# Optimization experiments

Measured on AMD Instinct MI355X. Metric: run time of the kernel, lower is better.

Reference implementation:

```python
import jax, jax.numpy as jnp
import numpy as np

N_NODES = 200_000
N_EVENTS = 50_000
MEM = 128
RAW = 64
TD = 64
HEADS = 2
DH = MEM // HEADS
EDGE_DIM = RAW + TD
MSG_IN = 2 * MEM + RAW + TD


def _time_enc(x, w, b):
    # PyG TimeEncoder: cos(Linear(t)) with Linear(1, time_dim)
    return jnp.cos(x[..., None] * w + b)


def setup_inputs() -> dict:
    key = jax.random.key(0)
    ks = jax.random.split(key, 30)

    def w(i, shape, scale=None):
        s = scale if scale is not None else 1.0 / np.sqrt(shape[-1])
        return jax.random.normal(ks[i], shape, jnp.float32) * s

    src = jax.random.randint(ks[0], (N_EVENTS,), 0, N_NODES)
    dst = jax.random.randint(ks[1], (N_EVENTS,), 0, N_NODES)
    t = jnp.sort(jax.random.uniform(ks[2], (N_EVENTS,), jnp.float32, 0.0, 1e4))
    return dict(
        memory=w(3, (N_NODES, MEM), 1.0),
        last_update=jnp.zeros((N_NODES,), jnp.float32),
        t=t,
        msg=w(4, (N_EVENTS, RAW), 1.0),
        src=src, dst=dst,
        time_w=w(5, (TD,), 1.0), time_b=w(6, (TD,), 1.0),
        gru_Wih=w(7, (3 * MEM, MSG_IN)), gru_bih=w(8, (3 * MEM,), 0.02),
        gru_Whh=w(9, (3 * MEM, MEM)), gru_bhh=w(10, (3 * MEM,), 0.02),
        Wq=w(11, (MEM, MEM)), bq=w(12, (MEM,), 0.02),
        Wk=w(13, (MEM, MEM)), bk=w(14, (MEM,), 0.02),
        Wv=w(15, (MEM, MEM)), bv=w(16, (MEM,), 0.02),
        We=w(17, (MEM, EDGE_DIM)),
        Wskip=w(18, (MEM, MEM)), bskip=w(19, (MEM,), 0.02),
        Wls=w(20, (MEM, MEM)), bls=w(21, (MEM,), 0.02),
        Wld=w(22, (MEM, MEM)), bld=w(23, (MEM,), 0.02),
        Wlf=w(24, (1, MEM)), blf=w(25, (1,), 0.02),
    )


def reference(memory, last_update, t, msg, src, dst, time_w, time_b,
              gru_Wih, gru_bih, gru_Whh, gru_bhh,
              Wq, bq, Wk, bk, Wv, bv, We, Wskip, bskip,
              Wls, bls, Wld, bld, Wlf, blf):
    N, D = memory.shape
    E = src.shape[0]
    # --- 1. IdentityMessage: raw store for src side and dst side of each event ---
    dt_s = t - last_update[src]
    dt_d = t - last_update[dst]
    m_s = jnp.concatenate([memory[src], memory[dst], msg, _time_enc(dt_s, time_w, time_b)], -1)
    m_d = jnp.concatenate([memory[dst], memory[src], msg, _time_enc(dt_d, time_w, time_b)], -1)
    all_msg = jnp.concatenate([m_s, m_d], 0)        # [2E, MSG_IN]
    all_id = jnp.concatenate([src, dst], 0)         # [2E]
    all_t = jnp.concatenate([t, t], 0)              # [2E]
    # --- 2. LastAggregator: keep the latest message per target node ---
    pos = jnp.arange(2 * E, dtype=jnp.int32)
    last_pos = jnp.full((N,), -1, jnp.int32).at[all_id].max(pos)
    is_last = last_pos[all_id] == pos               # [2E], exactly one True per touched node
    # --- 3. GRUCell memory update (computed per message, scattered for the last one) ---
    h = memory[all_id]
    gi = all_msg @ gru_Wih.T + gru_bih
    gh = h @ gru_Whh.T + gru_bhh
    ir, iz, i_n = jnp.split(gi, 3, -1)
    hr, hz, h_n = jnp.split(gh, 3, -1)
    r = jax.nn.sigmoid(ir + hr)
    zg = jax.nn.sigmoid(iz + hz)
    n = jnp.tanh(i_n + r * h_n)
    h_new = (1.0 - zg) * n + zg * h
    memory_new = memory.at[all_id].add(jnp.where(is_last[:, None], h_new - h, 0.0))
    last_update_new = last_update.at[all_id].max(jnp.where(is_last, all_t, -jnp.inf))
    # --- 4. GraphAttentionEmbedding: TransformerConv(heads=2, edge_dim) in eval mode ---
    rel_t = last_update_new[src] - t
    edge_attr = jnp.concatenate([_time_enc(rel_t, time_w, time_b), msg], -1)  # [E, EDGE_DIM]
    e_proj = edge_attr @ We.T                                                  # [E, MEM]
    q = (memory_new @ Wq.T + bq).reshape(N, HEADS, DH)
    k = (memory_new[src] @ Wk.T + bk + e_proj).reshape(E, HEADS, DH)
    v = (memory_new[src] @ Wv.T + bv + e_proj).reshape(E, HEADS, DH)
    logit = jnp.einsum('ehd,ehd->eh', q[dst], k) / np.sqrt(DH).astype(np.float32)
    mx = jnp.full((N, HEADS), -jnp.inf, memory.dtype).at[dst].max(logit)
    a = jnp.exp(logit - mx[dst])
    denom = jax.ops.segment_sum(a, dst, num_segments=N)
    attn = a / denom[dst]                                                      # segment softmax over incoming edges
    out = jnp.zeros((N, HEADS, DH), memory.dtype).at[dst].add(attn[..., None] * v)
    z = out.reshape(N, D) + memory_new @ Wskip.T + bskip                       # root/skip connection
    # --- 5. LinkPredictor on event endpoints ---
    hlp = jax.nn.relu(z[src] @ Wls.T + bls + z[dst] @ Wld.T + bld)
    return hlp @ Wlf.T + blf                                                   # [E, 1]
```

## Files before the change

### kernel.cpp

```cpp
#include <hip/hip_runtime.h>
#include <math.h>

#define NN 200000
#define NE 50000
#define D 128

#define WGRU_SZ  196608
#define WATTN_SZ 147456
#define WSKP_SZ  16384
#define WLINK_SZ 32768

__device__ __forceinline__ float frcp_(float x) { return __builtin_amdgcn_rcpf(x); }
__device__ __forceinline__ float fsig_(float x) { return frcp_(1.f + __expf(-x)); }
__device__ __forceinline__ float ftanh_(float x) {
    float xc = fminf(fmaxf(x, -15.f), 15.f);
    float t = __expf(2.f * xc);
    return (t - 1.f) * frcp_(t + 1.f);
}

__device__ __forceinline__ unsigned short f2bf(float f) {
    unsigned int u = __float_as_uint(f);
    u = (u + 0x7fffu + ((u >> 16) & 1u)) >> 16;
    return (unsigned short)u;
}
__device__ __forceinline__ float bf2f(unsigned short b) {
    return __uint_as_float(((unsigned int)b) << 16);
}

typedef short bf16x8 __attribute__((ext_vector_type(8)));
typedef float f32x4  __attribute__((ext_vector_type(4)));

__global__ void k_initprep(const float* __restrict__ Wih, const float* __restrict__ Whh,
                           const float* __restrict__ Wk, const float* __restrict__ Wv,
                           const float* __restrict__ Wq, const float* __restrict__ We,
                           const float* __restrict__ Wskip,
                           const float* __restrict__ Wls, const float* __restrict__ Wld,
                           const int* __restrict__ src, const int* __restrict__ dst,
                           unsigned short* __restrict__ wgru,
                           unsigned short* __restrict__ wattn,
                           unsigned short* __restrict__ wskp,
                           unsigned short* __restrict__ wlink,
                           int* __restrict__ last_pos, int* __restrict__ count) {
    int idx = blockIdx.x * 256 + threadIdx.x;
    if (idx == 0) *count = 0;
    if (idx < 2 * NE) {
        int id = (idx < NE) ? src[idx] : dst[idx - NE];
        atomicMax(&last_pos[id], idx + 1);
    }
    if (idx >= 49152 + 36864 + 4096 + 8192) return;
    float4 v;
    unsigned short* dstp;
    int ncopies, stride;
    if (idx < 49152) {
        int n = idx / 96;
        int c = (idx - n * 96) * 4;
        if (n < 384) {
            v = *(const float4*)&Wih[n * 384 + c];
            if (n < 256 && c < 128) {
                const float4 w2 = *(const float4*)&Whh[n * 128 + c];
                v.x += w2.x; v.y += w2.y; v.z += w2.z; v.w += w2.w;
            }
        } else {
            if (c >= 128) return;
            v = *(const float4*)&Whh[(n - 128) * 128 + c];
        }
        dstp = &wgru[n * 384 + c]; ncopies = 8; stride = WGRU_SZ;
    } else if (idx < 49152 + 36864) {
        int i2 = idx - 49152;
        int n = i2 / 96;
        int c = (i2 - n * 96) * 4;
        if (n < 256) {
            const float* Wm = (n < 128) ? Wk : Wv;
            int nn = n & 127;
            if (c < 128)       v = *(const float4*)&Wm[nn * 128 + c];
            else if (c < 256)  v = *(const float4*)&We[nn * 128 + (c - 128)];
            else return;
        } else {
            if (c < 256) return;
            v = *(const float4*)&Wq[(n - 256) * 128 + (c - 256)];
        }
        dstp = &wattn[n * 384 + c]; ncopies = 4; stride = WATTN_SZ;
    } else if (idx < 49152 + 36864 + 4096) {
        int i3 = idx - 49152 - 36864;
        int n = i3 / 32;
        int c = (i3 - n * 32) * 4;
        v = *(const float4*)&Wskip[n * 128 + c];
        dstp = &wskp[n * 128 + c]; ncopies = 8; stride = WSKP_SZ;
    } else {
        int i4 = idx - 49152 - 36864 - 4096;
        int n = i4 / 64;
        int c = (i4 - n * 64) * 4;
        if (c < 128) v = *(const float4*)&Wls[n * 128 + c];
        else         v = *(const float4*)&Wld[n * 128 + (c - 128)];
        dstp = &wlink[n * 256 + c]; ncopies = 4; stride = WLINK_SZ;
    }
    ushort4 b;
    b.x = f2bf(v.x); b.y = f2bf(v.y); b.z = f2bf(v.z); b.w = f2bf(v.w);
    for (int r = 0; r < ncopies; ++r)
        *(ushort4*)(dstp + (size_t)r * stride) = b;
}

__global__ void k_compact(const int* __restrict__ src, const int* __restrict__ dst,
                          const int* __restrict__ last_pos,
                          int* __restrict__ count, int* __restrict__ clist,
                          int* __restrict__ node2slot, int* __restrict__ head) {
    int i = blockIdx.x * blockDim.x + threadIdx.x;
    if (i < 2 * NE) {
        int id = (i < NE) ? src[i] : dst[i - NE];
        if (last_pos[id] == i + 1) {
            int s = atomicAdd(count, 1);
            clist[s] = i;
            node2slot[id] = s;
            head[s] = -1;
        }
    }
}

#define GMB 64
__global__ __launch_bounds__(512) void k_gru(
    const float* __restrict__ memp, const float* __restrict__ lup,
    const float* __restrict__ tp, const float* __restrict__ msgp,
    const int* __restrict__ srcp, const int* __restrict__ dstp,
    const float* __restrict__ twp, const float* __restrict__ tbp,
    const int* __restrict__ clist,
    const unsigned short* __restrict__ wgru_all,
    const float* __restrict__ bih, const float* __restrict__ bhh,
    const unsigned short* __restrict__ wskp_all, const float* __restrict__ bskip,
    const int* __restrict__ countp,
    unsigned short* __restrict__ mem_new, unsigned short* __restrict__ zbf,
    float* __restrict__ lu_new)
{
    __shared__ alignas(16) unsigned short Xs[64][392];
    __shared__ int sid[64], sother[64], se[64];
    __shared__ float sdt[64];
    int cnt = *countp;
    int base = blockIdx.x * GMB;
    if (base >= cnt) return;
    int tid = threadIdx.x;
    const unsigned short* __restrict__ wgru = wgru_all + (size_t)(blockIdx.x & 7) * WGRU_SZ;
    const unsigned short* __restrict__ wskp = wskp_all + (size_t)(blockIdx.x & 7) * WSKP_SZ;

    if (tid < 64) {
        int ii = base + tid;
        bool valid = ii < cnt;
        int iw = clist[valid ? ii : (cnt - 1)];
        int e = (iw < NE) ? iw : (iw - NE);
        int id    = (iw < NE) ? srcp[e] : dstp[e];
        int oth   = (iw < NE) ? dstp[e] : srcp[e];
        sid[tid] = id; sother[tid] = oth; se[tid] = e;
        float tt = tp[e];
        float lu = lup[id];
        sdt[tid] = tt - lu;
        if (valid) lu_new[id] = fmaxf(lu, tt);
    }
    __syncthreads();
    {
        int m = tid >> 3, li = tid & 7;
        int id = sid[m], oth = sother[m], e = se[m];
        float dt = sdt[m];
        #pragma unroll
        for (int j = 0; j < 12; ++j) {
            int c4 = li + 8 * j;
            float4 v;
            if (c4 < 32)      v = *(const float4*)&memp[id * D + c4 * 4];
            else if (c4 < 64) v = *(const float4*)&memp[oth * D + (c4 - 32) * 4];
            else if (c4 < 80) v = *(const float4*)&msgp[e * 64 + (c4 - 64) * 4];
            else {
                int c0 = (c4 - 80) * 4;
                v.x = cosf(dt * twp[c0 + 0] + tbp[c0 + 0]);
                v.y = cosf(dt * twp[c0 + 1] + tbp[c0 + 1]);
                v.z = cosf(dt * twp[c0 + 2] + tbp[c0 + 2]);
                v.w = cosf(dt * twp[c0 + 3] + tbp[c0 + 3]);
            }
            ushort4 b;
            b.x = f2bf(v.x); b.y = f2bf(v.y); b.z = f2bf(v.z); b.w = f2bf(v.w);
            *(ushort4*)&Xs[m][c4 * 4] = b;
        }
    }
    __syncthreads();

    int lane = tid & 63, w = tid >> 6;
    int q = lane >> 4, l15 = lane & 15;
    int q8 = q * 8, w16 = w * 16;

    f32x4 acc[4][4];
    #pragma unroll
    for (int mt = 0; mt < 4; ++mt)
        #pragma unroll
        for (int g = 0; g < 4; ++g)
            acc[mt][g] = (f32x4)(0.0f);

#define GRU_STEP(NG)                                                                      \
    {                                                                                     \
        bf16x8 a[4];                                                                      \
        _Pragma("unroll")                                                                 \
        for (int mt = 0; mt < 4; ++mt) a[mt] = *(const bf16x8*)&Xs[mt * 16 + l15][k0 + q8]; \
        _Pragma("unroll")                                                                 \
        for (int g = 0; g < NG; ++g) {                                                    \
            const bf16x8 b = *(const bf16x8*)&wgru[(g * 128 + w16 + l15) * 384 + k0 + q8]; \
            _Pragma("unroll")                                                             \
            for (int mt = 0; mt < 4; ++mt)                                                \
                acc[mt][g] = __builtin_amdgcn_mfma_f32_16x16x32_bf16(a[mt], b, acc[mt][g], 0, 0, 0); \
        }                                                                                 \
    }

    #pragma unroll 2
    for (int ks = 0; ks < 4; ++ks) { int k0 = ks * 32; GRU_STEP(4) }
    #pragma unroll 2
    for (int ks = 4; ks < 12; ++ks) { int k0 = ks * 32; GRU_STEP(3) }
#undef GRU_STEP

    float nval[4][4];
    {
        int c = w16 + l15;
        float br  = bih[c]       + bhh[c];
        float bz  = bih[128 + c] + bhh[128 + c];
        float bin = bih[256 + c];
        float bhn = bhh[256 + c];
        #pragma unroll
        for (int mt = 0; mt < 4; ++mt) {
            #pragma unroll
            for (int reg = 0; reg < 4; ++reg) {
                int m = mt * 16 + q * 4 + reg;
                float r  = fsig_(acc[mt][0][reg] + br);
                float zg = fsig_(acc[mt][1][reg] + bz);
                float n  = ftanh_(acc[mt][2][reg] + bin + r * (acc[mt][3][reg] + bhn));
                float hv = bf2f(Xs[m][c]);
                nval[mt][reg] = (1.f - zg) * n + zg * hv;
            }
        }
    }

    __syncthreads();
    {
        int c = w16 + l15;
        #pragma unroll
        for (int mt = 0; mt < 4; ++mt)
            #pragma unroll
            for (int reg = 0; reg < 4; ++reg)
                Xs[mt * 16 + q * 4 + reg][c] = f2bf(nval[mt][reg]);
    }
    __syncthreads();

    {
        #pragma unroll
        for (int j = 0; j < 2; ++j) {
            int ch = tid + 512 * j;
            int m = ch >> 4, c8 = ch & 15;
            *(uint4*)&mem_new[(size_t)(base + m) * D + c8 * 8] = *(const uint4*)&Xs[m][c8 * 8];
        }
    }

    f32x4 acc2[4];
    #pragma unroll
    for (int mt = 0; mt < 4; ++mt) acc2[mt] = (f32x4)(0.0f);
    #pragma unroll
    for (int ks = 0; ks < 4; ++ks) {
        int k0 = ks * 32;
        bf16x8 a[4];
        #pragma unroll
        for (int mt = 0; mt < 4; ++mt) a[mt] = *(const bf16x8*)&Xs[mt * 16 + l15][k0 + q8];
        const bf16x8 b = *(const bf16x8*)&wskp[(w16 + l15) * 128 + k0 + q8];
        #pragma unroll
        for (int mt = 0; mt < 4; ++mt)
            acc2[mt] = __builtin_amdgcn_mfma_f32_16x16x32_bf16(a[mt], b, acc2[mt], 0, 0, 0);
    }
    __syncthreads();
    {
        int ch = w16 + l15;
        float b = bskip[ch];
        #pragma unroll
        for (int mt = 0; mt < 4; ++mt)
            #pragma unroll
            for (int reg = 0; reg < 4; ++reg)
                Xs[mt * 16 + q * 4 + reg][ch] = f2bf(acc2[mt][reg] + b);
    }
    __syncthreads();
    {
        #pragma unroll
        for (int j = 0; j < 2; ++j) {
            int ch = tid + 512 * j;
            int m = ch >> 4, c8 = ch & 15;
            *(uint4*)&zbf[(size_t)(base + m) * D + c8 * 8] = *(const uint4*)&Xs[m][c8 * 8];
        }
    }
}

#define AMB 32
__global__ __launch_bounds__(256) void k_attnA(
    const int* __restrict__ srcp, const int* __restrict__ dstp,
    const float* __restrict__ tp, const float* __restrict__ msgp,
    const float* __restrict__ twp, const float* __restrict__ tbp,
    const float* __restrict__ lu_new, const int* __restrict__ node2slot,
    const unsigned short* __restrict__ mem_new,
    const unsigned short* __restrict__ wattn_all,
    const float* __restrict__ bq, const float* __restrict__ bk, const float* __restrict__ bv,
    unsigned short* __restrict__ vbuf, float* __restrict__ abuf,
    int* __restrict__ head, int* __restrict__ next)
{
    __shared__ alignas(16) unsigned short Xs[32][392];
    unsigned short (*kLb)[136] = (unsigned short(*)[136])(&Xs[0][0]);
    unsigned short (*qLb)[136] = (unsigned short(*)[136])(&Xs[0][0] + 4352);
    __shared__ float sa[AMB][2];
    __shared__ int sslot[AMB], sdslot[AMB];
    __shared__ float srel[AMB];
    int tid = threadIdx.x;
    int e0 = blockIdx.x * AMB;
    const unsigned short* __restrict__ wattn = wattn_all + (size_t)(blockIdx.x & 3) * WATTN_SZ;
    {
        int gid = blockIdx.x * 256 + tid;
        if (gid < NE) {
            int sl = node2slot[dstp[gid]];
            next[gid] = atomicExch(&head[sl], gid);
        }
    }
    if (tid < AMB) {
        int e = e0 + tid; if (e >= NE) e = NE - 1;
        int s = srcp[e], dd = dstp[e];
        sslot[tid]  = node2slot[s];
        sdslot[tid] = node2slot[dd];
        srel[tid] = lu_new[s] - tp[e];
    }
    __syncthreads();
    {
        int m = tid >> 3, li = tid & 7;
        int e = e0 + m; if (e >= NE) e = NE - 1;
        int ssl = sslot[m], dsl = sdslot[m];
        float rel = srel[m];
        uint4* xrow = (uint4*)&Xs[m][0];
        const uint4* srow = (const uint4*)&mem_new[(size_t)ssl * D];
        const uint4* drow = (const uint4*)&mem_new[(size_t)dsl * D];
        #pragma unroll
        for (int j = 0; j < 2; ++j) {
            xrow[li + 8 * j]      = srow[li + 8 * j];
            xrow[32 + li + 8 * j] = drow[li + 8 * j];
        }
        {
            int c0 = li * 8;
            ushort4 lo, hi;
            lo.x = f2bf(cosf(rel * twp[c0 + 0] + tbp[c0 + 0]));
            lo.y = f2bf(cosf(rel * twp[c0 + 1] + tbp[c0 + 1]));
            lo.z = f2bf(cosf(rel * twp[c0 + 2] + tbp[c0 + 2]));
            lo.w = f2bf(cosf(rel * twp[c0 + 3] + tbp[c0 + 3]));
            hi.x = f2bf(cosf(rel * twp[c0 + 4] + tbp[c0 + 4]));
            hi.y = f2bf(cosf(rel * twp[c0 + 5] + tbp[c0 + 5]));
            hi.z = f2bf(cosf(rel * twp[c0 + 6] + tbp[c0 + 6]));
            hi.w = f2bf(cosf(rel * twp[c0 + 7] + tbp[c0 + 7]));
            *(ushort4*)&Xs[m][128 + c0]     = lo;
            *(ushort4*)&Xs[m][128 + c0 + 4] = hi;
        }
        {
            float4 a = *(const float4*)&msgp[e * 64 + li * 8];
            float4 b = *(const float4*)&msgp[e * 64 + li * 8 + 4];
            ushort4 lo, hi;
            lo.x = f2bf(a.x); lo.y = f2bf(a.y); lo.z = f2bf(a.z); lo.w = f2bf(a.w);
            hi.x = f2bf(b.x); hi.y = f2bf(b.y); hi.z = f2bf(b.z); hi.w = f2bf(b.w);
            *(ushort4*)&Xs[m][192 + li * 8]     = lo;
            *(ushort4*)&Xs[m][192 + li * 8 + 4] = hi;
        }
    }
    __syncthreads();

    int lane = tid & 63, w = tid >> 6;
    int q = lane >> 4, l15 = lane & 15;
    int q8 = q * 8;

    f32x4 acc[2][6];
    #pragma unroll
    for (int mt = 0; mt < 2; ++mt)
        #pragma unroll
        for (int jj = 0; jj < 6; ++jj) acc[mt][jj] = (f32x4)(0.0f);

    #pragma unroll 2
    for (int ks = 0; ks < 8; ++ks) {
        int k0 = ks * 32;
        const bf16x8 a0 = *(const bf16x8*)&Xs[l15][k0 + q8];
        const bf16x8 a1 = *(const bf16x8*)&Xs[16 + l15][k0 + q8];
        #pragma unroll
        for (int jj = 0; jj < 4; ++jj) {
            int nt = w + 4 * jj;
            const bf16x8 b = *(const bf16x8*)&wattn[(nt * 16 + l15) * 384 + k0 + q8];
            acc[0][jj] = __builtin_amdgcn_mfma_f32_16x16x32_bf16(a0, b, acc[0][jj], 0, 0, 0);
            acc[1][jj] = __builtin_amdgcn_mfma_f32_16x16x32_bf16(a1, b, acc[1][jj], 0, 0, 0);
        }
    }
    #pragma unroll 2
    for (int ks = 8; ks < 12; ++ks) {
        int k0 = ks * 32;
        const bf16x8 a0 = *(const bf16x8*)&Xs[l15][k0 + q8];
        const bf16x8 a1 = *(const bf16x8*)&Xs[16 + l15][k0 + q8];
        #pragma unroll
        for (int jj = 4; jj < 6; ++jj) {
            int nt = w + 4 * jj;
            const bf16x8 b = *(const bf16x8*)&wattn[(nt * 16 + l15) * 384 + k0 + q8];
            acc[0][jj] = __builtin_amdgcn_mfma_f32_16x16x32_bf16(a0, b, acc[0][jj], 0, 0, 0);
            acc[1][jj] = __builtin_amdgcn_mfma_f32_16x16x32_bf16(a1, b, acc[1][jj], 0, 0, 0);
        }
    }

    __syncthreads();

    float vreg[2][2][4];
    #pragma unroll
    for (int jj = 0; jj < 6; ++jj) {
        int nt = w + 4 * jj;
        int gate = nt >> 3;
        int ch = (nt & 7) * 16 + l15;
        float bias = (gate == 0) ? bk[ch] : (gate == 1) ? bv[ch] : bq[ch];
        #pragma unroll
        for (int mt = 0; mt < 2; ++mt)
            #pragma unroll
            for (int reg = 0; reg < 4; ++reg) {
                int m = mt * 16 + q * 4 + reg;
                float val = acc[mt][jj][reg] + bias;
                if (gate == 0)      kLb[m][ch] = f2bf(val);
                else if (gate == 2) qLb[m][ch] = f2bf(val);
                else                vreg[jj - 2][mt][reg] = val;
            }
    }
    __syncthreads();
    #pragma unroll
    for (int pr = 0; pr < 16; ++pr) {
        int p2 = pr * 4 + w;
        int m = p2 >> 1, h = p2 & 1;
        float prod = bf2f(qLb[m][h * 64 + lane]) * bf2f(kLb[m][h * 64 + lane]);
        #pragma unroll
        for (int off = 32; off; off >>= 1) prod += __shfl_down(prod, off);
        if (lane == 0) {
            float a = __expf(prod * 0.125f);
            sa[m][h] = a;
            if (e0 + m < NE) abuf[(e0 + m) * 2 + h] = a;
        }
    }
    __syncthreads();
    {
        unsigned short (*vL)[136] = qLb;
        #pragma unroll
        for (int jv = 0; jv < 2; ++jv) {
            int ch = w * 16 + jv * 64 + l15;
            int h = jv;
            #pragma unroll
            for (int mt = 0; mt < 2; ++mt)
                #pragma unroll
                for (int reg = 0; reg < 4; ++reg) {
                    int m = mt * 16 + q * 4 + reg;
                    vL[m][ch] = f2bf(sa[m][h] * vreg[jv][mt][reg]);
                }
        }
        __syncthreads();
        #pragma unroll
        for (int j = 0; j < 2; ++j) {
            int chunk = tid + 256 * j;
            int row = chunk >> 4, c8 = chunk & 15;
            if (e0 + row < NE)
                *(uint4*)&vbuf[(size_t)(e0 + row) * D + c8 * 8] = *(const uint4*)&vL[row][c8 * 8];
        }
    }
}

__global__ __launch_bounds__(256) void k_gather(
    const int* __restrict__ countp, const int* __restrict__ head,
    const int* __restrict__ next, const float* __restrict__ abuf,
    const unsigned short* __restrict__ vbuf, unsigned short* __restrict__ zbf)
{
    int cnt = *countp;
    int slot = blockIdx.x * 32 + (threadIdx.x >> 3);
    if (slot >= cnt) return;
    int li = threadIdx.x & 7;
    int c0 = li * 16;
    int h = li >> 2;
    float vsum[16];
    #pragma unroll
    for (int j = 0; j < 16; ++j) vsum[j] = 0.f;
    float asum = 0.f;
    for (int e = head[slot]; e != -1; e = next[e]) {
        asum += abuf[e * 2 + h];
        uint4 v0 = *(const uint4*)&vbuf[(size_t)e * D + c0];
        uint4 v1 = *(const uint4*)&vbuf[(size_t)e * D + c0 + 8];
        const unsigned short* pv0 = (const unsigned short*)&v0;
        const unsigned short* pv1 = (const unsigned short*)&v1;
        #pragma unroll
        for (int j = 0; j < 8; ++j) { vsum[j] += bf2f(pv0[j]); vsum[8 + j] += bf2f(pv1[j]); }
    }
    if (asum > 0.f) {
        float rr = frcp_(asum);
        uint4 z0 = *(const uint4*)&zbf[(size_t)slot * D + c0];
        uint4 z1 = *(const uint4*)&zbf[(size_t)slot * D + c0 + 8];
        const unsigned short* pz0 = (const unsigned short*)&z0;
        const unsigned short* pz1 = (const unsigned short*)&z1;
        unsigned short o[16];
        #pragma unroll
        for (int j = 0; j < 8; ++j) {
            o[j]     = f2bf(bf2f(pz0[j]) + vsum[j] * rr);
            o[8 + j] = f2bf(bf2f(pz1[j]) + vsum[8 + j] * rr);
        }
        *(uint4*)&zbf[(size_t)slot * D + c0]     = *(const uint4*)&o[0];
        *(uint4*)&zbf[(size_t)slot * D + c0 + 8] = *(const uint4*)&o[8];
    }
}

__global__ __launch_bounds__(256) void k_link(
    const int* __restrict__ srcp, const int* __restrict__ dstp,
    const int* __restrict__ node2slot,
    const unsigned short* __restrict__ zbf,
    const unsigned short* __restrict__ wlink_all,
    const float* __restrict__ bls, const float* __restrict__ bld,
    const float* __restrict__ Wlf, const float* __restrict__ blf,
    float* __restrict__ outp)
{
    __shared__ alignas(16) unsigned short Xs[32][264];
    __shared__ int ssl[32], sdl[32];
    __shared__ float sred[32][4];
    int tid = threadIdx.x;
    int e0 = blockIdx.x * 32;
    const unsigned short* __restrict__ wlink = wlink_all + (size_t)(blockIdx.x & 3) * WLINK_SZ;
    if (tid < 32) {
        int e = e0 + tid; if (e >= NE) e = NE - 1;
        ssl[tid] = node2slot[srcp[e]];
        sdl[tid] = node2slot[dstp[e]];
    }
    __syncthreads();
    {
        int m = tid >> 3, li = tid & 7;
        uint4* xrow = (uint4*)&Xs[m][0];
        const uint4* srow = (const uint4*)&zbf[(size_t)ssl[m] * D];
        const uint4* drow = (const uint4*)&zbf[(size_t)sdl[m] * D];
        xrow[li]      = srow[li];
        xrow[li + 8]  = srow[li + 8];
        xrow[16 + li] = drow[li];
        xrow[24 + li] = drow[li + 8];
    }
    __syncthreads();

    int lane = tid & 63, w = tid >> 6;
    int q = lane >> 4, l15 = lane & 15;
    int q8 = q * 8;

    f32x4 acc[2][2];
    #pragma unroll
    for (int mt = 0; mt < 2; ++mt)
        #pragma unroll
        for (int jj = 0; jj < 2; ++jj) acc[mt][jj] = (f32x4)(0.0f);

    #pragma unroll
    for (int ks = 0; ks < 8; ++ks) {
        int k0 = ks * 32;
        const bf16x8 a0 = *(const bf16x8*)&Xs[l15][k0 + q8];
        const bf16x8 a1 = *(const bf16x8*)&Xs[16 + l15][k0 + q8];
        #pragma unroll
        for (int jj = 0; jj < 2; ++jj) {
            int nt = w + 4 * jj;
            const bf16x8 b = *(const bf16x8*)&wlink[(nt * 16 + l15) * 256 + k0 + q8];
            acc[0][jj] = __builtin_amdgcn_mfma_f32_16x16x32_bf16(a0, b, acc[0][jj], 0, 0, 0);
            acc[1][jj] = __builtin_amdgcn_mfma_f32_16x16x32_bf16(a1, b, acc[1][jj], 0, 0, 0);
        }
    }

    float p[2][4];
    #pragma unroll
    for (int mt = 0; mt < 2; ++mt)
        #pragma unroll
        for (int reg = 0; reg < 4; ++reg) p[mt][reg] = 0.f;
    #pragma unroll
    for (int jj = 0; jj < 2; ++jj) {
        int ch = (w + 4 * jj) * 16 + l15;
        float bias = bls[ch] + bld[ch];
        float wl = Wlf[ch];
        #pragma unroll
        for (int mt = 0; mt < 2; ++mt)
            #pragma unroll
            for (int reg = 0; reg < 4; ++reg)
                p[mt][reg] += fmaxf(acc[mt][jj][reg] + bias, 0.f) * wl;
    }
    #pragma unroll
    for (int mask = 1; mask < 16; mask <<= 1) {
        #pragma unroll
        for (int mt = 0; mt < 2; ++mt)
            #pragma unroll
            for (int reg = 0; reg < 4; ++reg)
                p[mt][reg] += __shfl_xor(p[mt][reg], mask);
    }
    if (l15 == 0) {
        #pragma unroll
        for (int mt = 0; mt < 2; ++mt)
            #pragma unroll
            for (int reg = 0; reg < 4; ++reg)
                sred[mt * 16 + q * 4 + reg][w] = p[mt][reg];
    }
    __syncthreads();
    if (tid < 32) {
        int e = e0 + tid;
        if (e < NE)
            outp[e] = sred[tid][0] + sred[tid][1] + sred[tid][2] + sred[tid][3] + blf[0];
    }
}

extern "C" void kernel_launch(void* const* d_in, const int* in_sizes, int n_in,
                              void* d_out, int out_size, void* d_ws, size_t ws_size,
                              hipStream_t stream)
{
    const float* memory      = (const float*)d_in[0];
    const float* last_update = (const float*)d_in[1];
    const float* t           = (const float*)d_in[2];
    const float* msg         = (const float*)d_in[3];
    const int*   src         = (const int*)d_in[4];
    const int*   dst         = (const int*)d_in[5];
    const float* time_w      = (const float*)d_in[6];
    const float* time_b      = (const float*)d_in[7];
    const float* gru_Wih     = (const float*)d_in[8];
    const float* gru_bih     = (const float*)d_in[9];
    const float* gru_Whh     = (const float*)d_in[10];
    const float* gru_bhh     = (const float*)d_in[11];
    const float* Wq          = (const float*)d_in[12];
    const float* bq          = (const float*)d_in[13];
    const float* Wk          = (const float*)d_in[14];
    const float* bk          = (const float*)d_in[15];
    const float* Wv          = (const float*)d_in[16];
    const float* bv          = (const float*)d_in[17];
    const float* We          = (const float*)d_in[18];
    const float* Wskip       = (const float*)d_in[19];
    const float* bskip       = (const float*)d_in[20];
    const float* Wls         = (const float*)d_in[21];
    const float* bls         = (const float*)d_in[22];
    const float* Wld         = (const float*)d_in[23];
    const float* bld         = (const float*)d_in[24];
    const float* Wlf         = (const float*)d_in[25];
    const float* blf         = (const float*)d_in[26];
    float* outp = (float*)d_out;

    char* ws = (char*)d_ws;
    int*   last_pos  = (int*)  (ws + 0);
    int*   node2slot = (int*)  (ws + 800000);
    float* lu_new    = (float*)(ws + 1600000);
    int*   count     = (int*)  (ws + 2400000);
    int*   clist     = (int*)  (ws + 2400016);
    unsigned short* wgru    = (unsigned short*)(ws + 79624592);
    unsigned short* wattn   = (unsigned short*)(ws + 82770320);
    unsigned short* wskp    = (unsigned short*)(ws + 83949968);
    unsigned short* wlink   = (unsigned short*)(ws + 84212112);
    unsigned short* mem_new = (unsigned short*)(ws + 84474256);
    unsigned short* zbf     = (unsigned short*)(ws + 110082448);
    unsigned short* vbuf    = (unsigned short*)(ws + 135690640);
    float* abuf = (float*)(ws + 148490640);
    int*   head = (int*)  (ws + 148890640);
    int*   next = (int*)  (ws + 149290768);

    k_initprep<<<(2 * NE + 255) / 256, 256, 0, stream>>>(
                 gru_Wih, gru_Whh, Wk, Wv, Wq, We, Wskip, Wls, Wld, src, dst,
                 wgru, wattn, wskp, wlink, last_pos, count);
    k_compact <<<(2 * NE + 255) / 256, 256, 0, stream>>>(src, dst, last_pos, count,
                 clist, node2slot, head);
    k_gru     <<<(2 * NE + GMB - 1) / GMB, 512, 0, stream>>>(memory, last_update, t, msg,
                 src, dst, time_w, time_b, clist, wgru, gru_bih, gru_bhh,
                 wskp, bskip, count, mem_new, zbf, lu_new);
    k_attnA   <<<(NE + AMB - 1) / AMB, 256, 0, stream>>>(src, dst, t, msg, time_w, time_b,
                 lu_new, node2slot, mem_new, wattn, bq, bk, bv, vbuf, abuf, head, next);
    k_gather  <<<(2 * NE + 31) / 32, 256, 0, stream>>>(count, head, next, abuf, vbuf, zbf);
    k_link    <<<(NE + 31) / 32, 256, 0, stream>>>(src, dst, node2slot, zbf,
                 wlink, bls, bld, Wlf, blf, outp);
}
```

Before: 385.3 us.

## Precompute per-slot metadata and bf16 msg, widen attention tile to 64 edges

k_compact now writes a packed int4 per compacted slot (event, other node, dt, id) and the lu_new update, so k_gru no longer does a serial metadata phase with an extra barrier. msg is converted to bf16 once in k_initprep and both k_gru and k_attnA copy it directly. k_attnA is restructured to 64 edges per 512-thread block, with each wave owning one 16-channel column per gate, which increases A-fragment reuse per weight load. The cost is an extra msg conversion pass, a larger launch grid for initprep, and more LDS per attention block, which may lower occupancy.

```diff
diff --git a/kernel.cpp b/kernel.cpp
--- a/kernel.cpp
+++ b/kernel.cpp
@@ -9,6 +9,9 @@
 #define WATTN_SZ 147456
 #define WSKP_SZ  16384
 #define WLINK_SZ 32768
+
+#define CVT0 98304
+#define MSGB_V4 800000
 
 __device__ __forceinline__ float frcp_(float x) { return __builtin_amdgcn_rcpf(x); }
 __device__ __forceinline__ float fsig_(float x) { return frcp_(1.f + __expf(-x)); }
@@ -36,10 +39,12 @@
                            const float* __restrict__ Wskip,
                            const float* __restrict__ Wls, const float* __restrict__ Wld,
                            const int* __restrict__ src, const int* __restrict__ dst,
+                           const float* __restrict__ msg,
                            unsigned short* __restrict__ wgru,
                            unsigned short* __restrict__ wattn,
                            unsigned short* __restrict__ wskp,
                            unsigned short* __restrict__ wlink,
+                           unsigned short* __restrict__ msgb,
                            int* __restrict__ last_pos, int* __restrict__ count) {
     int idx = blockIdx.x * 256 + threadIdx.x;
     if (idx == 0) *count = 0;
@@ -47,7 +52,16 @@
         int id = (idx < NE) ? src[idx] : dst[idx - NE];
         atomicMax(&last_pos[id], idx + 1);
     }
-    if (idx >= 49152 + 36864 + 4096 + 8192) return;
+    if (idx >= CVT0) {
+        int j = idx - CVT0;
+        if (j < MSGB_V4) {
+            float4 v = ((const float4*)msg)[j];
+            ushort4 b;
+            b.x = f2bf(v.x); b.y = f2bf(v.y); b.z = f2bf(v.z); b.w = f2bf(v.w);
+            ((ushort4*)msgb)[j] = b;
+        }
+        return;
+    }
     float4 v;
     unsigned short* dstp;
     int ncopies, stride;
@@ -102,37 +116,40 @@
 
 __global__ void k_compact(const int* __restrict__ src, const int* __restrict__ dst,
                           const int* __restrict__ last_pos,
-                          int* __restrict__ count, int* __restrict__ clist,
-                          int* __restrict__ node2slot, int* __restrict__ head) {
+                          const float* __restrict__ tp, const float* __restrict__ lup,
+                          int* __restrict__ count, int* __restrict__ node2slot,
+                          int* __restrict__ head,
+                          int4* __restrict__ slot_aux,
+                          float* __restrict__ lu_new) {
     int i = blockIdx.x * blockDim.x + threadIdx.x;
-    if (i < 2 * NE) {
-        int id = (i < NE) ? src[i] : dst[i - NE];
-        if (last_pos[id] == i + 1) {
-            int s = atomicAdd(count, 1);
-            clist[s] = i;
-            node2slot[id] = s;
-            head[s] = -1;
-        }
-    }
+    if (i >= 2 * NE) return;
+    int e  = (i < NE) ? i : i - NE;
+    int id = (i < NE) ? src[e] : dst[e];
+    if (last_pos[id] != i + 1) return;
+    int s = atomicAdd(count, 1);
+    node2slot[id] = s;
+    head[s] = -1;
+    int oth = (i < NE) ? dst[e] : src[e];
+    float tt = tp[e];
+    float lu = lup[id];
+    lu_new[id] = fmaxf(lu, tt);
+    int4 aux; aux.x = e; aux.y = oth; aux.z = __float_as_int(tt - lu); aux.w = id;
+    slot_aux[s] = aux;
 }
 
 #define GMB 64
 __global__ __launch_bounds__(512) void k_gru(
-    const float* __restrict__ memp, const float* __restrict__ lup,
-    const float* __restrict__ tp, const float* __restrict__ msgp,
-    const int* __restrict__ srcp, const int* __restrict__ dstp,
+    const float* __restrict__ memp,
+    const unsigned short* __restrict__ msgb,
     const float* __restrict__ twp, const float* __restrict__ tbp,
-    const int* __restrict__ clist,
+    const int4* __restrict__ slot_aux,
     const unsigned short* __restrict__ wgru_all,
     const float* __restrict__ bih, const float* __restrict__ bhh,
     const unsigned short* __restrict__ wskp_all, const float* __restrict__ bskip,
     const int* __restrict__ countp,
-    unsigned short* __restrict__ mem_new, unsigned short* __restrict__ zbf,
-    float* __restrict__ lu_new)
+    unsigned short* __restrict__ mem_new, unsigned short* __restrict__ zbf)
 {
     __shared__ alignas(16) unsigned short Xs[64][392];
-    __shared__ int sid[64], sother[64], se[64];
-    __shared__ float sdt[64];
     int cnt = *countp;
     int base = blockIdx.x * GMB;
     if (base >= cnt) return;
@@ -140,42 +157,36 @@
     const unsigned short* __restrict__ wgru = wgru_all + (size_t)(blockIdx.x & 7) * WGRU_SZ;
     const unsigned short* __restrict__ wskp = wskp_all + (size_t)(blockIdx.x & 7) * WSKP_SZ;
 
-    if (tid < 64) {
-        int ii = base + tid;
-        bool valid = ii < cnt;
-        int iw = clist[valid ? ii : (cnt - 1)];
-        int e = (iw < NE) ? iw : (iw - NE);
-        int id    = (iw < NE) ? srcp[e] : dstp[e];
-        int oth   = (iw < NE) ? dstp[e] : srcp[e];
-        sid[tid] = id; sother[tid] = oth; se[tid] = e;
-        float tt = tp[e];
-        float lu = lup[id];
-        sdt[tid] = tt - lu;
-        if (valid) lu_new[id] = fmaxf(lu, tt);
-    }
-    __syncthreads();
     {
         int m = tid >> 3, li = tid & 7;
-        int id = sid[m], oth = sother[m], e = se[m];
-        float dt = sdt[m];
-        #pragma unroll
-        for (int j = 0; j < 12; ++j) {
-            int c4 = li + 8 * j;
-            float4 v;
-            if (c4 < 32)      v = *(const float4*)&memp[id * D + c4 * 4];
-            else if (c4 < 64) v = *(const float4*)&memp[oth * D + (c4 - 32) * 4];
-            else if (c4 < 80) v = *(const float4*)&msgp[e * 64 + (c4 - 64) * 4];
-            else {
-                int c0 = (c4 - 80) * 4;
-                v.x = cosf(dt * twp[c0 + 0] + tbp[c0 + 0]);
-                v.y = cosf(dt * twp[c0 + 1] + tbp[c0 + 1]);
-                v.z = cosf(dt * twp[c0 + 2] + tbp[c0 + 2]);
-                v.w = cosf(dt * twp[c0 + 3] + tbp[c0 + 3]);
-            }
+        int ii = base + m; if (ii >= cnt) ii = cnt - 1;
+        const int4 aux = slot_aux[ii];
+        int e = aux.x, oth = aux.y, id = aux.w;
+        float dt = __int_as_float(aux.z);
+        const float4* idr  = (const float4*)(memp + (size_t)id  * D);
+        const float4* othr = (const float4*)(memp + (size_t)oth * D);
+        #pragma unroll
+        for (int s4 = 0; s4 < 4; ++s4) {
+            float4 v = idr[li + 8 * s4];
             ushort4 b;
             b.x = f2bf(v.x); b.y = f2bf(v.y); b.z = f2bf(v.z); b.w = f2bf(v.w);
-            *(ushort4*)&Xs[m][c4 * 4] = b;
-        }
+            *(ushort4*)&Xs[m][(li + 8 * s4) * 4] = b;
+            float4 v2 = othr[li + 8 * s4];
+            ushort4 b2;
+            b2.x = f2bf(v2.x); b2.y = f2bf(v2.y); b2.z = f2bf(v2.z); b2.w = f2bf(v2.w);
+            *(ushort4*)&Xs[m][128 + (li + 8 * s4) * 4] = b2;
+        }
+        *(uint4*)&Xs[m][256 + li * 8] = *(const uint4*)&msgb[e * 64 + li * 8];
+        int c0 = li * 8;
+        float cv[8];
+        #pragma unroll
+        for (int k = 0; k < 8; ++k)
+            cv[k] = cosf(dt * twp[c0 + k] + tbp[c0 + k]);
+        ushort4 t0, t1;
+        t0.x = f2bf(cv[0]); t0.y = f2bf(cv[1]); t0.z = f2bf(cv[2]); t0.w = f2bf(cv[3]);
+        t1.x = f2bf(cv[4]); t1.y = f2bf(cv[5]); t1.z = f2bf(cv[6]); t1.w = f2bf(cv[7]);
+        *(ushort4*)&Xs[m][320 + c0]     = t0;
+        *(ushort4*)&Xs[m][320 + c0 + 4] = t1;
     }
     __syncthreads();
 
@@ -286,10 +297,10 @@
     }
 }
 
-#define AMB 32
-__global__ __launch_bounds__(256) void k_attnA(
+#define AMB 64
+__global__ __launch_bounds__(512) void k_attnA(
     const int* __restrict__ srcp, const int* __restrict__ dstp,
-    const float* __restrict__ tp, const float* __restrict__ msgp,
+    const float* __restrict__ tp, const unsigned short* __restrict__ msgb,
     const float* __restrict__ twp, const float* __restrict__ tbp,
     const float* __restrict__ lu_new, const int* __restrict__ node2slot,
     const unsigned short* __restrict__ mem_new,
@@ -298,9 +309,9 @@
     unsigned short* __restrict__ vbuf, float* __restrict__ abuf,
     int* __restrict__ head, int* __restrict__ next)
 {
-    __shared__ alignas(16) unsigned short Xs[32][392];
+    __shared__ alignas(16) unsigned short Xs[64][392];
     unsigned short (*kLb)[136] = (unsigned short(*)[136])(&Xs[0][0]);
-    unsigned short (*qLb)[136] = (unsigned short(*)[136])(&Xs[0][0] + 4352);
+    unsigned short (*qLb)[136] = (unsigned short(*)[136])(&Xs[0][0] + 8704);
     __shared__ float sa[AMB][2];
     __shared__ int sslot[AMB], sdslot[AMB];
     __shared__ float srel[AMB];
@@ -308,7 +319,7 @@
     int e0 = blockIdx.x * AMB;
     const unsigned short* __restrict__ wattn = wattn_all + (size_t)(blockIdx.x & 3) * WATTN_SZ;
     {
-        int gid = blockIdx.x * 256 + tid;
+        int gid = blockIdx.x * 512 + tid;
         if (gid < NE) {
             int sl = node2slot[dstp[gid]];
             next[gid] = atomicExch(&head[sl], gid);
@@ -349,15 +360,7 @@
             *(ushort4*)&Xs[m][128 + c0]     = lo;
             *(ushort4*)&Xs[m][128 + c0 + 4] = hi;
         }
-        {
-            float4 a = *(const float4*)&msgp[e * 64 + li * 8];
-            float4 b = *(const float4*)&msgp[e * 64 + li * 8 + 4];
-            ushort4 lo, hi;
-            lo.x = f2bf(a.x); lo.y = f2bf(a.y); lo.z = f2bf(a.z); lo.w = f2bf(a.w);
-            hi.x = f2bf(b.x); hi.y = f2bf(b.y); hi.z = f2bf(b.z); hi.w = f2bf(b.w);
-            *(ushort4*)&Xs[m][192 + li * 8]     = lo;
-            *(ushort4*)&Xs[m][192 + li * 8 + 4] = hi;
-        }
+        *(uint4*)&Xs[m][192 + li * 8] = *(const uint4*)&msgb[e * 64 + li * 8];
     }
     __syncthreads();
 
@@ -365,63 +368,64 @@
     int q = lane >> 4, l15 = lane & 15;
     int q8 = q * 8;
 
-    f32x4 acc[2][6];
-    #pragma unroll
-    for (int mt = 0; mt < 2; ++mt)
-        #pragma unroll
-        for (int jj = 0; jj < 6; ++jj) acc[mt][jj] = (f32x4)(0.0f);
+    f32x4 acc[4][3];
+    #pragma unroll
+    for (int mt = 0; mt < 4; ++mt)
+        #pragma unroll
+        for (int jj = 0; jj < 3; ++jj) acc[mt][jj] = (f32x4)(0.0f);
 
     #pragma unroll 2
     for (int ks = 0; ks < 8; ++ks) {
         int k0 = ks * 32;
-        const bf16x8 a0 = *(const bf16x8*)&Xs[l15][k0 + q8];
-        const bf16x8 a1 = *(const bf16x8*)&Xs[16 + l15][k0 + q8];
-        #pragma unroll
-        for (int jj = 0; jj < 4; ++jj) {
-            int nt = w + 4 * jj;
+        bf16x8 a[4];
+        #pragma unroll
+        for (int mt = 0; mt < 4; ++mt) a[mt] = *(const bf16x8*)&Xs[mt * 16 + l15][k0 + q8];
+        #pragma unroll
+        for (int jj = 0; jj < 2; ++jj) {
+            int nt = w + 8 * jj;
             const bf16x8 b = *(const bf16x8*)&wattn[(nt * 16 + l15) * 384 + k0 + q8];
-            acc[0][jj] = __builtin_amdgcn_mfma_f32_16x16x32_bf16(a0, b, acc[0][jj], 0, 0, 0);
-            acc[1][jj] = __builtin_amdgcn_mfma_f32_16x16x32_bf16(a1, b, acc[1][jj], 0, 0, 0);
+            #pragma unroll
+            for (int mt = 0; mt < 4; ++mt)
+                acc[mt][jj] = __builtin_amdgcn_mfma_f32_16x16x32_bf16(a[mt], b, acc[mt][jj], 0, 0, 0);
         }
     }
     #pragma unroll 2
     for (int ks = 8; ks < 12; ++ks) {
         int k0 = ks * 32;
-        const bf16x8 a0 = *(const bf16x8*)&Xs[l15][k0 + q8];
-        const bf16x8 a1 = *(const bf16x8*)&Xs[16 + l15][k0 + q8];
-        #pragma unroll
-        for (int jj = 4; jj < 6; ++jj) {
-            int nt = w + 4 * jj;
-            const bf16x8 b = *(const bf16x8*)&wattn[(nt * 16 + l15) * 384 + k0 + q8];
-            acc[0][jj] = __builtin_amdgcn_mfma_f32_16x16x32_bf16(a0, b, acc[0][jj], 0, 0, 0);
-            acc[1][jj] = __builtin_amdgcn_mfma_f32_16x16x32_bf16(a1, b, acc[1][jj], 0, 0, 0);
-        }
-    }
-
-    __syncthreads();
-
-    float vreg[2][2][4];
-    #pragma unroll
-    for (int jj = 0; jj < 6; ++jj) {
-        int nt = w + 4 * jj;
-        int gate = nt >> 3;
-        int ch = (nt & 7) * 16 + l15;
-        float bias = (gate == 0) ? bk[ch] : (gate == 1) ? bv[ch] : bq[ch];
-        #pragma unroll
-        for (int mt = 0; mt < 2; ++mt)
-            #pragma unroll
-            for (int reg = 0; reg < 4; ++reg) {
-                int m = mt * 16 + q * 4 + reg;
-                float val = acc[mt][jj][reg] + bias;
-                if (gate == 0)      kLb[m][ch] = f2bf(val);
-                else if (gate == 2) qLb[m][ch] = f2bf(val);
-                else                vreg[jj - 2][mt][reg] = val;
-            }
+        bf16x8 a[4];
+        #pragma unroll
+        for (int mt = 0; mt < 4; ++mt) a[mt] = *(const bf16x8*)&Xs[mt * 16 + l15][k0 + q8];
+        int nt = 16 + w;
+        const bf16x8 b = *(const bf16x8*)&wattn[(nt * 16 + l15) * 384 + k0 + q8];
+        #pragma unroll
+        for (int mt = 0; mt < 4; ++mt)
+            acc[mt][2] = __builtin_amdgcn_mfma_f32_16x16x32_bf16(a[mt], b, acc[mt][2], 0, 0, 0);
+    }
+
+    __syncthreads();
+
+    float vreg[4][4];
+    {
+        int ch = w * 16 + l15;
+        #pragma unroll
+        for (int jj = 0; jj < 3; ++jj) {
+            float bias = (jj == 0) ? bk[ch] : (jj == 1) ? bv[ch] : bq[ch];
+            #pragma unroll
+            for (int mt = 0; mt < 4; ++mt)
+                #pragma unroll
+                for (int reg = 0; reg < 4; ++reg) {
+                    int m = mt * 16 + q * 4 + reg;
+                    float val = acc[mt][jj][reg] + bias;
+                    if (jj == 0)      kLb[m][ch] = f2bf(val);
+                    else if (jj == 2) qLb[m][ch] = f2bf(val);
+                    else              vreg[mt][reg] = val;
+                }
+        }
     }
     __syncthreads();
     #pragma unroll
     for (int pr = 0; pr < 16; ++pr) {
-        int p2 = pr * 4 + w;
+        int p2 = pr * 8 + w;
         int m = p2 >> 1, h = p2 & 1;
         float prod = bf2f(qLb[m][h * 64 + lane]) * bf2f(kLb[m][h * 64 + lane]);
         #pragma unroll
@@ -435,22 +439,19 @@
     __syncthreads();
     {
         unsigned short (*vL)[136] = qLb;
-        #pragma unroll
-        for (int jv = 0; jv < 2; ++jv) {
-            int ch = w * 16 + jv * 64 + l15;
-            int h = jv;
-            #pragma unroll
-            for (int mt = 0; mt < 2; ++mt)
-                #pragma unroll
-                for (int reg = 0; reg < 4; ++reg) {
-                    int m = mt * 16 + q * 4 + reg;
-                    vL[m][ch] = f2bf(sa[m][h] * vreg[jv][mt][reg]);
-                }
-        }
+        int ch = w * 16 + l15;
+        int h = w >> 2;
+        #pragma unroll
+        for (int mt = 0; mt < 4; ++mt)
+            #pragma unroll
+            for (int reg = 0; reg < 4; ++reg) {
+                int m = mt * 16 + q * 4 + reg;
+                vL[m][ch] = f2bf(sa[m][h] * vreg[mt][reg]);
+            }
         __syncthreads();
         #pragma unroll
         for (int j = 0; j < 2; ++j) {
-            int chunk = tid + 256 * j;
+            int chunk = tid + 512 * j;
             int row = chunk >> 4, c8 = chunk & 15;
             if (e0 + row < NE)
                 *(uint4*)&vbuf[(size_t)(e0 + row) * D + c8 * 8] = *(const uint4*)&vL[row][c8 * 8];
@@ -499,6 +500,7 @@
     }
 }
 
+#define ALB 32
 __global__ __launch_bounds__(256) void k_link(
     const int* __restrict__ srcp, const int* __restrict__ dstp,
     const int* __restrict__ node2slot,
@@ -512,9 +514,9 @@
     __shared__ int ssl[32], sdl[32];
     __shared__ float sred[32][4];
     int tid = threadIdx.x;
-    int e0 = blockIdx.x * 32;
+    int e0 = blockIdx.x * ALB;
     const unsigned short* __restrict__ wlink = wlink_all + (size_t)(blockIdx.x & 3) * WLINK_SZ;
-    if (tid < 32) {
+    if (tid < ALB) {
         int e = e0 + tid; if (e >= NE) e = NE - 1;
         ssl[tid] = node2slot[srcp[e]];
         sdl[tid] = node2slot[dstp[e]];
@@ -588,7 +590,7 @@
                 sred[mt * 16 + q * 4 + reg][w] = p[mt][reg];
     }
     __syncthreads();
-    if (tid < 32) {
+    if (tid < ALB) {
         int e = e0 + tid;
         if (e < NE)
             outp[e] = sred[tid][0] + sred[tid][1] + sred[tid][2] + sred[tid][3] + blf[0];
@@ -633,29 +635,29 @@
     int*   node2slot = (int*)  (ws + 800000);
     float* lu_new    = (float*)(ws + 1600000);
     int*   count     = (int*)  (ws + 2400000);
-    int*   clist     = (int*)  (ws + 2400016);
-    unsigned short* wgru    = (unsigned short*)(ws + 79624592);
-    unsigned short* wattn   = (unsigned short*)(ws + 82770320);
-    unsigned short* wskp    = (unsigned short*)(ws + 83949968);
-    unsigned short* wlink   = (unsigned short*)(ws + 84212112);
-    unsigned short* mem_new = (unsigned short*)(ws + 84474256);
-    unsigned short* zbf     = (unsigned short*)(ws + 110082448);
-    unsigned short* vbuf    = (unsigned short*)(ws + 135690640);
-    float* abuf = (float*)(ws + 148490640);
-    int*   head = (int*)  (ws + 148890640);
-    int*   next = (int*)  (ws + 149290768);
-
-    k_initprep<<<(2 * NE + 255) / 256, 256, 0, stream>>>(
-                 gru_Wih, gru_Whh, Wk, Wv, Wq, We, Wskip, Wls, Wld, src, dst,
-                 wgru, wattn, wskp, wlink, last_pos, count);
-    k_compact <<<(2 * NE + 255) / 256, 256, 0, stream>>>(src, dst, last_pos, count,
-                 clist, node2slot, head);
-    k_gru     <<<(2 * NE + GMB - 1) / GMB, 512, 0, stream>>>(memory, last_update, t, msg,
-                 src, dst, time_w, time_b, clist, wgru, gru_bih, gru_bhh,
-                 wskp, bskip, count, mem_new, zbf, lu_new);
-    k_attnA   <<<(NE + AMB - 1) / AMB, 256, 0, stream>>>(src, dst, t, msg, time_w, time_b,
+    int4*  slot_aux  = (int4*) (ws + 2400016);
+    unsigned short* msgb    = (unsigned short*)(ws + 4000528);
+    unsigned short* wgru    = (unsigned short*)(ws + 10400528);
+    unsigned short* wattn   = (unsigned short*)(ws + 13546256);
+    unsigned short* wskp    = (unsigned short*)(ws + 14725904);
+    unsigned short* wlink   = (unsigned short*)(ws + 14988048);
+    unsigned short* mem_new = (unsigned short*)(ws + 15250192);
+    unsigned short* zbf     = (unsigned short*)(ws + 40858384);
+    unsigned short* vbuf    = (unsigned short*)(ws + 66466576);
+    float* abuf = (float*)(ws + 79266576);
+    int*   head = (int*)  (ws + 79666576);
+    int*   next = (int*)  (ws + 80066704);
+
+    k_initprep<<<(CVT0 + MSGB_V4 + 255) / 256, 256, 0, stream>>>(
+                 gru_Wih, gru_Whh, Wk, Wv, Wq, We, Wskip, Wls, Wld, src, dst, msg,
+                 wgru, wattn, wskp, wlink, msgb, last_pos, count);
+    k_compact <<<(2 * NE + 255) / 256, 256, 0, stream>>>(src, dst, last_pos,
+                 t, last_update, count, node2slot, head, slot_aux, lu_new);
+    k_gru     <<<(2 * NE + GMB - 1) / GMB, 512, 0, stream>>>(memory, msgb, time_w, time_b,
+                 slot_aux, wgru, gru_bih, gru_bhh, wskp, bskip, count, mem_new, zbf);
+    k_attnA   <<<(NE + AMB - 1) / AMB, 512, 0, stream>>>(src, dst, t, msgb, time_w, time_b,
                  lu_new, node2slot, mem_new, wattn, bq, bk, bv, vbuf, abuf, head, next);
     k_gather  <<<(2 * NE + 31) / 32, 256, 0, stream>>>(count, head, next, abuf, vbuf, zbf);
-    k_link    <<<(NE + 31) / 32, 256, 0, stream>>>(src, dst, node2slot, zbf,
+    k_link    <<<(NE + ALB - 1) / ALB, 256, 0, stream>>>(src, dst, node2slot, zbf,
                  wlink, bls, bld, Wlf, blf, outp);
 }
```

After: 373.6 us. -3.0%, faster.
